# Kernel tuning notes

Measured on AMD Instinct MI355X. Metric: run time of the kernel, lower is better.

## Reference

```python
import jax, jax.numpy as jnp
import numpy as np

N = 4096      # number of nodes
C = 8         # channels (w1..w8 in source)
IN_DIM = 256  # input feature dim
D = 64        # per-channel dim (c_dim)
OUT = 128     # out_dim
ITERS = 4     # routing iterations
BETA = 1.0    # temperature
DENSITY = 0.01


def _l2norm(x):
    # tf.nn.l2_normalize along last axis with eps=1e-12
    return x * jax.lax.rsqrt(jnp.maximum(jnp.sum(x * x, axis=-1, keepdims=True), 1e-12))


def setup_inputs() -> dict:
    key = jax.random.key(0)
    k0, k1, k2, k3, k4, k5 = jax.random.split(key, 6)
    features = jax.random.normal(k0, (N, IN_DIM), dtype=jnp.float32)
    # sparse-ish 0/1 adjacency stored densely (as in the original model)
    adj = (jax.random.uniform(k1, (N, N)) < DENSITY).astype(jnp.float32)
    W = jax.random.normal(k2, (C, IN_DIM, D), dtype=jnp.float32)    # w1..w8 stacked
    b = jax.random.normal(k3, (C, 1, D), dtype=jnp.float32)         # b1..b8 stacked
    W_o = jax.random.normal(k4, (C * D, OUT), dtype=jnp.float32)
    bias = jax.random.normal(k5, (1, OUT), dtype=jnp.float32)
    return {"features": features, "adj": adj, "W": W, "b": b, "W_o": W_o, "bias": bias}


def reference(features, adj, W, b, W_o, bias):
    mask = adj > 0  # [N, N]
    # per-channel projection + l2 normalize: z[c] = l2norm(features @ w[c] + b[c])
    z = _l2norm(jnp.einsum('ni,cid->cnd', features, W) + b)  # [C, N, D]
    for _ in range(ITERS):
        # dense per-channel attention (XX^T), masked by adjacency
        A = jnp.einsum('cnd,cmd->cnm', z, z)                 # [C, N, N]
        A = jnp.where(mask[None], A, 0.0) / BETA
        # softmax across channels at each (i, j), then re-mask
        A = jax.nn.softmax(A, axis=0)
        A = jnp.where(mask[None], A, 0.0)
        # aggregate + residual + l2 normalize
        z = _l2norm(z + jnp.einsum('cnm,cmd->cnd', A, z))
    # concat channels along feature axis: [N, C*D]
    h = jnp.transpose(z, (1, 0, 2)).reshape(N, C * D)
    # (dropout skipped: stochastic op, identity in the deterministic reference)
    return h @ W_o + bias
```

## Files before the change

### kernel.cpp

```cpp
#include <hip/hip_runtime.h>
#include <hip/hip_bf16.h>

#define N_NODES 4096
#define C_CH    8
#define IN_DIM  256
#define D_DIM   64
#define CD      512
#define OUT_DIM 128
#define ITERS   4
#define STRIDE  128

typedef __hip_bfloat16 bf16;
typedef short short8 __attribute__((ext_vector_type(8)));
typedef float floatx4 __attribute__((ext_vector_type(4)));
typedef unsigned uintx4 __attribute__((ext_vector_type(4)));
typedef unsigned short ushortx4 __attribute__((ext_vector_type(4)));

__device__ __forceinline__ float bf2f(bf16 x) { return __bfloat162float(x); }

__device__ __forceinline__ unsigned f2b_rne(float x) {
    unsigned u = __float_as_uint(x);
    return (u + 0x7FFFu + ((u >> 16) & 1u)) >> 16;
}
__device__ __forceinline__ unsigned pack2bf(float a, float b) {
    return f2b_rne(a) | (f2b_rne(b) << 16);
}
__device__ __forceinline__ void unpack2(unsigned v, float& a, float& b) {
    a = __uint_as_float(v << 16);
    b = __uint_as_float(v & 0xFFFF0000u);
}
__device__ __forceinline__ short8 as_s8(uint4 u) {
    union { uint4 a; short8 b; } x; x.a = u; return x.b;
}

template<int CTRL>
__device__ __forceinline__ float dpp_add(float x) {
    int yi = __builtin_amdgcn_update_dpp(0, __float_as_int(x), CTRL, 0xF, 0xF, true);
    return x + __int_as_float(yi);
}

__device__ __forceinline__ bool wave_detect(const unsigned* __restrict__ feat_u) {
    int lane = threadIdx.x & 63;
    unsigned u = feat_u[lane];
    int e = (u >> 7) & 0xFF;
    int vote = (e >= 0x68 && e <= 0x86) ? 1 : 0;
    #pragma unroll
    for (int off = 32; off; off >>= 1) vote += __shfl_xor(vote, off);
    return vote >= 32;
}

__global__ __launch_bounds__(256) void stage_a(
        const void* __restrict__ feat, const void* __restrict__ W,
        const void* __restrict__ Wo,
        unsigned short* __restrict__ Wt, unsigned short* __restrict__ Wo_t) {
    bool isbf = wave_detect((const unsigned*)feat);
    int bx = blockIdx.x, t = threadIdx.x;
    if (bx < 8) {
        __shared__ __align__(16) unsigned short lt[IN_DIM * D_DIM];
        int c = bx;
        if (isbf) {
            const uint4* p = (const uint4*)((const unsigned short*)W + (size_t)c * IN_DIM * D_DIM);
            #pragma unroll
            for (int i = 0; i < 8; i++) {
                int idx = t + i * 256;
                *(uint4*)&lt[idx * 8] = p[idx];
            }
        } else {
            const float4* p = (const float4*)((const float*)W + (size_t)c * IN_DIM * D_DIM);
            #pragma unroll
            for (int i = 0; i < 16; i++) {
                int idx = t + i * 256;
                float4 f = p[idx];
                uint2 v = make_uint2(pack2bf(f.x, f.y), pack2bf(f.z, f.w));
                *(uint2*)&lt[idx * 4] = v;
            }
        }
        __syncthreads();
        uint4* wt4 = (uint4*)Wt;
        #pragma unroll
        for (int i = 0; i < 8; i++) {
            int j = t + i * 256;
            int d = j >> 5, seg = j & 31;
            int k0 = seg * 8;
            unsigned short v[8];
            #pragma unroll
            for (int k = 0; k < 8; k++) v[k] = lt[(k0 + k) * D_DIM + d];
            uint4 o;
            o.x = v[0] | ((unsigned)v[1] << 16);
            o.y = v[2] | ((unsigned)v[3] << 16);
            o.z = v[4] | ((unsigned)v[5] << 16);
            o.w = v[6] | ((unsigned)v[7] << 16);
            wt4[(c * 64 + d) * 32 + seg] = o;
        }
    } else {
        int base = (bx - 8) * 1024 + t * 4;
        #pragma unroll
        for (int q = 0; q < 4; q++) {
            int idx = base + q;
            int k = idx >> 7, n = idx & 127;
            unsigned short v;
            if (isbf) v = ((const unsigned short*)Wo)[idx];
            else      v = (unsigned short)f2b_rne(((const float*)Wo)[idx]);
            Wo_t[n * CD + k] = v;
        }
    }
}

__global__ __launch_bounds__(256) void stage_b(
        const void* __restrict__ feat, const void* __restrict__ adj,
        const void* __restrict__ b, const unsigned short* __restrict__ Wt,
        unsigned* __restrict__ zbf, int* __restrict__ deg,
        unsigned short* __restrict__ col_buf) {
    bool isbf = wave_detect((const unsigned*)feat);
    int bx = blockIdx.x, t = threadIdx.x;
    int w = t >> 6, lane = t & 63;
    __shared__ __align__(16) unsigned short zt[16 * CD];

    if (bx < 256) {
        int r0 = bx * 16;
        int n0 = w * 128;
        int m = lane & 15, quad = lane >> 4;
        int row = r0 + m;
        floatx4 acc[8];
        #pragma unroll
        for (int j = 0; j < 8; j++) acc[j] = (floatx4){0.f, 0.f, 0.f, 0.f};
        const uint4* wt4 = (const uint4*)Wt;

        if (isbf) {
            const uint4* a4 = (const uint4*)feat + (size_t)row * 32 + quad;
            #pragma unroll
            for (int k0 = 0; k0 < 8; k0++) {
                short8 a = as_s8(a4[k0 * 4]);
                #pragma unroll
                for (int j = 0; j < 8; j++) {
                    int col = n0 + j * 16 + m;
                    short8 bb = as_s8(wt4[col * 32 + k0 * 4 + quad]);
                    acc[j] = __builtin_amdgcn_mfma_f32_16x16x32_bf16(a, bb, acc[j], 0, 0, 0);
                }
            }
        } else {
            const float4* a4 = (const float4*)feat + (size_t)row * 64 + quad * 2;
            #pragma unroll
            for (int k0 = 0; k0 < 8; k0++) {
                float4 f0 = a4[k0 * 8], f1 = a4[k0 * 8 + 1];
                uint4 au;
                au.x = pack2bf(f0.x, f0.y); au.y = pack2bf(f0.z, f0.w);
                au.z = pack2bf(f1.x, f1.y); au.w = pack2bf(f1.z, f1.w);
                short8 a = as_s8(au);
                #pragma unroll
                for (int j = 0; j < 8; j++) {
                    int col = n0 + j * 16 + m;
                    short8 bb = as_s8(wt4[col * 32 + k0 * 4 + quad]);
                    acc[j] = __builtin_amdgcn_mfma_f32_16x16x32_bf16(a, bb, acc[j], 0, 0, 0);
                }
            }
        }

        float pre[8][4];
        #pragma unroll
        for (int j = 0; j < 8; j++) {
            int col = n0 + j * 16 + m;
            float bb = isbf ? bf2f(((const bf16*)b)[col]) : ((const float*)b)[col];
            #pragma unroll
            for (int r = 0; r < 4; r++) pre[j][r] = acc[j][r] + bb;
        }
        #pragma unroll
        for (int ch = 0; ch < 2; ch++) {
            float ss[4];
            #pragma unroll
            for (int r = 0; r < 4; r++) {
                float s = 0.f;
                #pragma unroll
                for (int jj = 0; jj < 4; jj++) {
                    float v = pre[ch * 4 + jj][r];
                    s = fmaf(v, v, s);
                }
                ss[r] = s;
            }
            #pragma unroll
            for (int off = 1; off < 16; off <<= 1) {
                #pragma unroll
                for (int r = 0; r < 4; r++) ss[r] += __shfl_xor(ss[r], off);
            }
            #pragma unroll
            for (int r = 0; r < 4; r++) {
                float sc = __builtin_amdgcn_rsqf(fmaxf(ss[r], 1e-12f));
                int lrow = quad * 4 + r;
                #pragma unroll
                for (int jj = 0; jj < 4; jj++) {
                    int j = ch * 4 + jj;
                    int col = n0 + j * 16 + m;
                    zt[lrow * CD + col] = (unsigned short)f2b_rne(pre[j][r] * sc);
                }
            }
        }
        __syncthreads();
        const uint4* zt4 = (const uint4*)zt;
        uint4* z4 = (uint4*)zbf;
        #pragma unroll
        for (int i = 0; i < 4; i++) {
            int j = t + i * 256;
            int lrow = j >> 6, seg = j & 63;
            z4[(size_t)(r0 + lrow) * 64 + seg] = zt4[j];
        }
    } else {
        int i = (bx - 256) * 4 + w;
        int base_out = i * STRIDE;
        int running = 0;
        int nch = isbf ? 8 : 16;
        for (int ch = 0; ch < nch; ch++) {
            unsigned bits = 0;
            int j0, nelem;
            if (isbf) {
                const uint4* p = (const uint4*)((const unsigned short*)adj + (size_t)i * N_NODES);
                uint4 u = p[ch * 64 + lane];
                j0 = (ch * 64 + lane) * 8; nelem = 8;
                unsigned short h[8] = {
                    (unsigned short)(u.x & 0xFFFF), (unsigned short)(u.x >> 16),
                    (unsigned short)(u.y & 0xFFFF), (unsigned short)(u.y >> 16),
                    (unsigned short)(u.z & 0xFFFF), (unsigned short)(u.z >> 16),
                    (unsigned short)(u.w & 0xFFFF), (unsigned short)(u.w >> 16)};
                #pragma unroll
                for (int k = 0; k < 8; k++)
                    if ((h[k] & 0x8000) == 0 && h[k] != 0) bits |= (1u << k);
            } else {
                const float4* p = (const float4*)((const float*)adj + (size_t)i * N_NODES);
                float4 f = p[ch * 64 + lane];
                j0 = (ch * 64 + lane) * 4; nelem = 4;
                if (f.x > 0.f) bits |= 1u;
                if (f.y > 0.f) bits |= 2u;
                if (f.z > 0.f) bits |= 4u;
                if (f.w > 0.f) bits |= 8u;
            }
            int cnt = __popc(bits);
            int sc = cnt;
            #pragma unroll
            for (int off = 1; off < 64; off <<= 1) {
                int v = __shfl_up(sc, off);
                if (lane >= off) sc += v;
            }
            int tot = __shfl(sc, 63);
            int pos = base_out + running + (sc - cnt);
            for (int k = 0; k < nelem; k++) {
                if ((bits >> k) & 1u) {
                    if (pos < base_out + STRIDE) col_buf[pos] = (unsigned short)(j0 + k);
                    pos++;
                }
            }
            running += tot;
        }
        if (lane == 0) deg[i] = (running < STRIDE) ? running : STRIDE;
    }
}

__device__ __forceinline__ void edge_step(const float zil2[8], float acc[8], uint4 u) {
    float vj[8];
    unpack2(u.x, vj[0], vj[1]);
    unpack2(u.y, vj[2], vj[3]);
    unpack2(u.z, vj[4], vj[5]);
    unpack2(u.w, vj[6], vj[7]);
    float p = 0.f;
    #pragma unroll
    for (int k = 0; k < 8; k++) p = fmaf(zil2[k], vj[k], p);
    p = dpp_add<0xB1>(p);
    p = dpp_add<0x4E>(p);
    p = dpp_add<0x141>(p);
    float ex = __builtin_amdgcn_exp2f(p);
    float s = dpp_add<0x128>(ex);
    s += __shfl_xor(s, 16);
    s += __shfl_xor(s, 32);
    float wgt = ex * __builtin_amdgcn_rcpf(s);
    #pragma unroll
    for (int k = 0; k < 8; k++) acc[k] = fmaf(wgt, vj[k], acc[k]);
}

__device__ __forceinline__ void finish_norm(float acc[8], float zi[8]) {
    float ss = 0.f;
    #pragma unroll
    for (int k = 0; k < 8; k++) ss = fmaf(acc[k], acc[k], ss);
    ss = dpp_add<0xB1>(ss);
    ss = dpp_add<0x4E>(ss);
    ss = dpp_add<0x141>(ss);
    float sc = __builtin_amdgcn_rsqf(fmaxf(ss, 1e-12f));
    #pragma unroll
    for (int k = 0; k < 8; k++) zi[k] = acc[k] * sc;
}

__global__ __launch_bounds__(256, 8) void route_iter(
        const unsigned* __restrict__ bin_u, unsigned* __restrict__ bot,
        const int* __restrict__ deg, const unsigned short* __restrict__ col_buf) {
    const float LOG2E = 1.4426950408889634f;
    int t = threadIdx.x;
    int w = t >> 6, lane = t & 63;
    int local = w >> 1;
    int half  = w & 1;
    int node = blockIdx.x * 2 + local;
    int g = lane >> 3, s = lane & 7;

    __shared__ __align__(16) unsigned short s_cols[2 * STRIDE];
    __shared__ __align__(16) float s_acc[2][CD];
    if (t < 128) {
        ((unsigned*)s_cols)[t] =
            ((const unsigned*)(col_buf + (size_t)blockIdx.x * (2 * STRIDE)))[t];
    }
    int dg = deg[node];
    __syncthreads();
    const unsigned short* mycols = s_cols + local * STRIDE;

    int frag = g * 32 + s * 4;
    unsigned fragb = (unsigned)frag << 2;

    uint4 uown = *(const uint4*)(bin_u + (size_t)node * 256 + frag);
    float zi[8], zil2[8], acc[8];
    unpack2(uown.x, zi[0], zi[1]); unpack2(uown.y, zi[2], zi[3]);
    unpack2(uown.z, zi[4], zi[5]); unpack2(uown.w, zi[6], zi[7]);
    #pragma unroll
    for (int k = 0; k < 8; k++) {
        zil2[k] = zi[k] * LOG2E;
        acc[k] = half ? 0.f : zi[k];
    }

    int h0 = ((dg >> 1) + 7) & ~7;
    if (h0 > dg) h0 = dg;
    int e   = half ? h0 : 0;
    int end = half ? dg : h0;

    const char* bin = (const char*)bin_u;
    for (; e + 3 < end; e += 4) {
        ushortx4 js = *(const ushortx4*)&mycols[e];
        uint4 u0 = *(const uint4*)(bin + (((unsigned)js.x << 10) + fragb));
        uint4 u1 = *(const uint4*)(bin + (((unsigned)js.y << 10) + fragb));
        uint4 u2 = *(const uint4*)(bin + (((unsigned)js.z << 10) + fragb));
        uint4 u3 = *(const uint4*)(bin + (((unsigned)js.w << 10) + fragb));
        edge_step(zil2, acc, u0);
        edge_step(zil2, acc, u1);
        edge_step(zil2, acc, u2);
        edge_step(zil2, acc, u3);
    }
    for (; e < end; e++) {
        unsigned j0 = mycols[e];
        uint4 u0 = *(const uint4*)(bin + ((j0 << 10) + fragb));
        edge_step(zil2, acc, u0);
    }

    int flat = g * D_DIM + s * 8;
    if (half) {
        *(float4*)&s_acc[local][flat]     = make_float4(acc[0], acc[1], acc[2], acc[3]);
        *(float4*)&s_acc[local][flat + 4] = make_float4(acc[4], acc[5], acc[6], acc[7]);
    }
    __syncthreads();
    if (!half) {
        float4 p0 = *(const float4*)&s_acc[local][flat];
        float4 p1 = *(const float4*)&s_acc[local][flat + 4];
        acc[0] += p0.x; acc[1] += p0.y; acc[2] += p0.z; acc[3] += p0.w;
        acc[4] += p1.x; acc[5] += p1.y; acc[6] += p1.z; acc[7] += p1.w;

        finish_norm(acc, zi);

        uintx4 ob;
        ob.x = pack2bf(zi[0], zi[1]); ob.y = pack2bf(zi[2], zi[3]);
        ob.z = pack2bf(zi[4], zi[5]); ob.w = pack2bf(zi[6], zi[7]);
        __builtin_nontemporal_store(
            ob, (uintx4*)(bot + (size_t)node * 256 + frag));
    }
}

__global__ __launch_bounds__(256) void out_gemm_mfma(
        const unsigned* __restrict__ zbf, const unsigned* __restrict__ wot_u,
        const void* __restrict__ bias, void* __restrict__ out,
        const void* __restrict__ feat) {
    bool isbf = wave_detect((const unsigned*)feat);
    int w = threadIdx.x >> 6, lane = threadIdx.x & 63;
    int r0 = blockIdx.x * 32 + (w & 1) * 16;
    int n0 = (w >> 1) * 64;
    int m = lane & 15, quad = lane >> 4;

    floatx4 acc0 = {0.f, 0.f, 0.f, 0.f}, acc1 = acc0, acc2 = acc0, acc3 = acc0;
    const unsigned* ap  = zbf   + (size_t)(r0 + m) * 256 + quad * 4;
    const unsigned* bp0 = wot_u + (size_t)(n0 + m) * 256 + quad * 4;
    const unsigned* bp1 = bp0 + 16 * 256;
    const unsigned* bp2 = bp0 + 32 * 256;
    const unsigned* bp3 = bp0 + 48 * 256;

    #pragma unroll
    for (int k0 = 0; k0 < 256; k0 += 16) {
        short8 a  = as_s8(*(const uint4*)(ap  + k0));
        short8 b0 = as_s8(*(const uint4*)(bp0 + k0));
        short8 b1 = as_s8(*(const uint4*)(bp1 + k0));
        short8 b2 = as_s8(*(const uint4*)(bp2 + k0));
        short8 b3 = as_s8(*(const uint4*)(bp3 + k0));
        acc0 = __builtin_amdgcn_mfma_f32_16x16x32_bf16(a, b0, acc0, 0, 0, 0);
        acc1 = __builtin_amdgcn_mfma_f32_16x16x32_bf16(a, b1, acc1, 0, 0, 0);
        acc2 = __builtin_amdgcn_mfma_f32_16x16x32_bf16(a, b2, acc2, 0, 0, 0);
        acc3 = __builtin_amdgcn_mfma_f32_16x16x32_bf16(a, b3, acc3, 0, 0, 0);
    }

    float accs[4][4] = {
        {acc0[0], acc0[1], acc0[2], acc0[3]},
        {acc1[0], acc1[1], acc1[2], acc1[3]},
        {acc2[0], acc2[1], acc2[2], acc2[3]},
        {acc3[0], acc3[1], acc3[2], acc3[3]}};
    #pragma unroll
    for (int c = 0; c < 4; c++) {
        int col = n0 + c * 16 + m;
        float bb = isbf ? bf2f(((const bf16*)bias)[col]) : ((const float*)bias)[col];
        #pragma unroll
        for (int r = 0; r < 4; r++) {
            int row = r0 + quad * 4 + r;
            float v = accs[c][r] + bb;
            size_t oi = (size_t)row * OUT_DIM + col;
            if (isbf) ((bf16*)out)[oi] = __float2bfloat16(v);
            else      ((float*)out)[oi] = v;
        }
    }
}

extern "C" void kernel_launch(void* const* d_in, const int* in_sizes, int n_in,
                              void* d_out, int out_size, void* d_ws, size_t ws_size,
                              hipStream_t stream) {
    const void* feat = d_in[0];
    const void* adj  = d_in[1];
    const void* W    = d_in[2];
    const void* b    = d_in[3];
    const void* Wo   = d_in[4];
    const void* bias = d_in[5];

    char* ws = (char*)d_ws;
    unsigned*       zbf_a   = (unsigned*)ws;
    unsigned*       zbf_b   = (unsigned*)(ws + (4u << 20));
    unsigned short* Wt      = (unsigned short*)(ws + (8u << 20));
    unsigned short* Wo_t    = (unsigned short*)(ws + (8u << 20) + (256u << 10));
    int*            deg     = (int*)(ws + (8u << 20) + (512u << 10));
    unsigned short* col_buf = (unsigned short*)(ws + (9u << 20));

    stage_a<<<72, 256, 0, stream>>>(feat, W, Wo, Wt, Wo_t);
    stage_b<<<1280, 256, 0, stream>>>(feat, adj, b, Wt, zbf_a, deg, col_buf);

    unsigned* bin = zbf_a;
    unsigned* bot = zbf_b;
    for (int it = 0; it < ITERS; it++) {
        route_iter<<<N_NODES / 2, 256, 0, stream>>>(bin, bot, deg, col_buf);
        unsigned* tb = bin; bin = bot; bot = tb;
    }

    out_gemm_mfma<<<N_NODES / 32, 256, 0, stream>>>(zbf_a, (const unsigned*)Wo_t,
                                                    bias, d_out, feat);
}
```

Measured before the change: 206.6 us.

## Fuse four routing iterations into one persistent kernel with a grid barrier

Replaces the four per-iteration route_iter launches with a single persistent kernel of 512 blocks. Each wave owns two nodes and runs all iterations, writing each iteration's output to its own buffer with write-through stores and meeting other blocks at a two-level atomic grid barrier. It drops the split of each node's edges across two waves and the shared-memory reduction between them, so each wave now walks a node's full edge list by itself. This removes launch gaps and the extra per-block reduction, but it relies on all blocks being co-resident, adds spin-wait cost at the barrier, and leaves less parallelism per node.

Result: slower. 222.1 us (+7.5%).

```diff
diff --git a/kernel.cpp b/kernel.cpp
--- a/kernel.cpp
+++ b/kernel.cpp
@@ -10,6 +10,16 @@
 #define ITERS   4
 #define STRIDE  128
 
+#define Z_STRIDE   (4u << 20)
+#define WT_OFF     (20u << 20)
+#define WOT_OFF    ((20u << 20) + (256u << 10))
+#define DEG_OFF    ((20u << 20) + (512u << 10))
+#define COL_OFF    (21u << 20)
+#define BAR_OFF    (22u << 20)
+
+#define RBLOCKS    512
+#define RGROUPS    32
+
 typedef __hip_bfloat16 bf16;
 typedef short short8 __attribute__((ext_vector_type(8)));
 typedef float floatx4 __attribute__((ext_vector_type(4)));
@@ -52,9 +62,15 @@
 __global__ __launch_bounds__(256) void stage_a(
         const void* __restrict__ feat, const void* __restrict__ W,
         const void* __restrict__ Wo,
-        unsigned short* __restrict__ Wt, unsigned short* __restrict__ Wo_t) {
+        unsigned short* __restrict__ Wt, unsigned short* __restrict__ Wo_t,
+        unsigned* __restrict__ bar) {
+    int bx = blockIdx.x, t = threadIdx.x;
+    if (bx == 72) {
+        #pragma unroll
+        for (int i = 0; i < 8; i++) bar[t + i * 256] = 0u;
+        return;
+    }
     bool isbf = wave_detect((const unsigned*)feat);
-    int bx = blockIdx.x, t = threadIdx.x;
     if (bx < 8) {
         __shared__ __align__(16) unsigned short lt[IN_DIM * D_DIM];
         int c = bx;
@@ -286,47 +302,16 @@
     for (int k = 0; k < 8; k++) zi[k] = acc[k] * sc;
 }
 
-__global__ __launch_bounds__(256, 8) void route_iter(
-        const unsigned* __restrict__ bin_u, unsigned* __restrict__ bot,
-        const int* __restrict__ deg, const unsigned short* __restrict__ col_buf) {
+__device__ __forceinline__ void route_node(
+        float zi[8], const unsigned short* mycols, int dg,
+        const char* bin, char* bout, int node, unsigned fragb, bool writethrough) {
     const float LOG2E = 1.4426950408889634f;
-    int t = threadIdx.x;
-    int w = t >> 6, lane = t & 63;
-    int local = w >> 1;
-    int half  = w & 1;
-    int node = blockIdx.x * 2 + local;
-    int g = lane >> 3, s = lane & 7;
-
-    __shared__ __align__(16) unsigned short s_cols[2 * STRIDE];
-    __shared__ __align__(16) float s_acc[2][CD];
-    if (t < 128) {
-        ((unsigned*)s_cols)[t] =
-            ((const unsigned*)(col_buf + (size_t)blockIdx.x * (2 * STRIDE)))[t];
-    }
-    int dg = deg[node];
-    __syncthreads();
-    const unsigned short* mycols = s_cols + local * STRIDE;
-
-    int frag = g * 32 + s * 4;
-    unsigned fragb = (unsigned)frag << 2;
-
-    uint4 uown = *(const uint4*)(bin_u + (size_t)node * 256 + frag);
-    float zi[8], zil2[8], acc[8];
-    unpack2(uown.x, zi[0], zi[1]); unpack2(uown.y, zi[2], zi[3]);
-    unpack2(uown.z, zi[4], zi[5]); unpack2(uown.w, zi[6], zi[7]);
-    #pragma unroll
-    for (int k = 0; k < 8; k++) {
-        zil2[k] = zi[k] * LOG2E;
-        acc[k] = half ? 0.f : zi[k];
-    }
-
-    int h0 = ((dg >> 1) + 7) & ~7;
-    if (h0 > dg) h0 = dg;
-    int e   = half ? h0 : 0;
-    int end = half ? dg : h0;
-
-    const char* bin = (const char*)bin_u;
-    for (; e + 3 < end; e += 4) {
+    float zil2[8], acc[8];
+    #pragma unroll
+    for (int k = 0; k < 8; k++) { zil2[k] = zi[k] * LOG2E; acc[k] = zi[k]; }
+
+    int e = 0;
+    for (; e + 3 < dg; e += 4) {
         ushortx4 js = *(const ushortx4*)&mycols[e];
         uint4 u0 = *(const uint4*)(bin + (((unsigned)js.x << 10) + fragb));
         uint4 u1 = *(const uint4*)(bin + (((unsigned)js.y << 10) + fragb));
@@ -337,31 +322,95 @@
         edge_step(zil2, acc, u2);
         edge_step(zil2, acc, u3);
     }
-    for (; e < end; e++) {
+    for (; e < dg; e++) {
         unsigned j0 = mycols[e];
         uint4 u0 = *(const uint4*)(bin + ((j0 << 10) + fragb));
         edge_step(zil2, acc, u0);
     }
 
-    int flat = g * D_DIM + s * 8;
-    if (half) {
-        *(float4*)&s_acc[local][flat]     = make_float4(acc[0], acc[1], acc[2], acc[3]);
-        *(float4*)&s_acc[local][flat + 4] = make_float4(acc[4], acc[5], acc[6], acc[7]);
-    }
+    finish_norm(acc, zi);
+
+    uintx4 ob;
+    ob.x = pack2bf(zi[0], zi[1]); ob.y = pack2bf(zi[2], zi[3]);
+    ob.z = pack2bf(zi[4], zi[5]); ob.w = pack2bf(zi[6], zi[7]);
+    char* p = bout + ((size_t)node << 10) + fragb;
+    if (writethrough) {
+        unsigned long long addr = (unsigned long long)(uintptr_t)p;
+        asm volatile("global_store_dwordx4 %0, %1, off sc0 sc1"
+                     :: "v"(addr), "v"(ob) : "memory");
+    } else {
+        *(uintx4*)p = ob;
+    }
+}
+
+__global__ __launch_bounds__(256, 2) void route_fused(
+        unsigned* __restrict__ zbase, const int* __restrict__ deg,
+        const unsigned short* __restrict__ col_buf, unsigned* __restrict__ bar) {
+    int t = threadIdx.x;
+    int w = t >> 6, lane = t & 63;
+    int b = blockIdx.x;
+    int g = lane >> 3, s = lane & 7;
+    int nA = b * 8 + w;
+    int nB = b * 8 + 4 + w;
+
+    __shared__ __align__(16) unsigned short s_cols[8 * STRIDE];
+    {
+        const unsigned* src = (const unsigned*)(col_buf + (size_t)b * 8 * STRIDE);
+        ((unsigned*)s_cols)[t]       = src[t];
+        ((unsigned*)s_cols)[t + 256] = src[t + 256];
+    }
+    int dgA = deg[nA], dgB = deg[nB];
     __syncthreads();
-    if (!half) {
-        float4 p0 = *(const float4*)&s_acc[local][flat];
-        float4 p1 = *(const float4*)&s_acc[local][flat + 4];
-        acc[0] += p0.x; acc[1] += p0.y; acc[2] += p0.z; acc[3] += p0.w;
-        acc[4] += p1.x; acc[5] += p1.y; acc[6] += p1.z; acc[7] += p1.w;
-
-        finish_norm(acc, zi);
-
-        uintx4 ob;
-        ob.x = pack2bf(zi[0], zi[1]); ob.y = pack2bf(zi[2], zi[3]);
-        ob.z = pack2bf(zi[4], zi[5]); ob.w = pack2bf(zi[6], zi[7]);
-        __builtin_nontemporal_store(
-            ob, (uintx4*)(bot + (size_t)node * 256 + frag));
+    const unsigned short* colsA = s_cols + w * STRIDE;
+    const unsigned short* colsB = s_cols + (4 + w) * STRIDE;
+
+    int frag = g * 32 + s * 4;
+    unsigned fragb = (unsigned)frag << 2;
+
+    uint4 ua = *(const uint4*)((const char*)zbase + ((size_t)nA << 10) + fragb);
+    uint4 ub = *(const uint4*)((const char*)zbase + ((size_t)nB << 10) + fragb);
+    float ziA[8], ziB[8];
+    unpack2(ua.x, ziA[0], ziA[1]); unpack2(ua.y, ziA[2], ziA[3]);
+    unpack2(ua.z, ziA[4], ziA[5]); unpack2(ua.w, ziA[6], ziA[7]);
+    unpack2(ub.x, ziB[0], ziB[1]); unpack2(ub.y, ziB[2], ziB[3]);
+    unpack2(ub.z, ziB[4], ziB[5]); unpack2(ub.w, ziB[6], ziB[7]);
+
+    for (int it = 0; it < ITERS; it++) {
+        const char* bin = (const char*)zbase + (size_t)it * Z_STRIDE;
+        char* bout = (char*)zbase + (size_t)(it + 1) * Z_STRIDE;
+        bool wt = (it != ITERS - 1);
+
+        route_node(ziA, colsA, dgA, bin, bout, nA, fragb, wt);
+        route_node(ziB, colsB, dgB, bin, bout, nB, fragb, wt);
+
+        if (it != ITERS - 1) {
+            __syncthreads();
+            if (t == 0) {
+                unsigned r1 = __hip_atomic_fetch_add(
+                        &bar[(b >> 4) * 32], 1u,
+                        __ATOMIC_RELAXED, __HIP_MEMORY_SCOPE_AGENT);
+                if ((r1 & 15u) == 15u) {
+                    unsigned r2 = __hip_atomic_fetch_add(
+                            &bar[RGROUPS * 32], 1u,
+                            __ATOMIC_RELAXED, __HIP_MEMORY_SCOPE_AGENT);
+                    if ((r2 & (RGROUPS - 1u)) == RGROUPS - 1u) {
+                        __hip_atomic_store(&bar[(RGROUPS + 1) * 32],
+                                           r2 / RGROUPS + 1u,
+                                           __ATOMIC_RELAXED,
+                                           __HIP_MEMORY_SCOPE_AGENT);
+                    }
+                }
+                unsigned target = (unsigned)(it + 1);
+                int tries = 0;
+                while (__hip_atomic_load(&bar[(RGROUPS + 1) * 32],
+                                         __ATOMIC_RELAXED,
+                                         __HIP_MEMORY_SCOPE_AGENT) < target) {
+                    __builtin_amdgcn_s_sleep(2);
+                    if (++tries > (1 << 18)) break;
+                }
+            }
+            __syncthreads();
+        }
     }
 }
 
@@ -426,23 +475,18 @@
     const void* bias = d_in[5];
 
     char* ws = (char*)d_ws;
-    unsigned*       zbf_a   = (unsigned*)ws;
-    unsigned*       zbf_b   = (unsigned*)(ws + (4u << 20));
-    unsigned short* Wt      = (unsigned short*)(ws + (8u << 20));
-    unsigned short* Wo_t    = (unsigned short*)(ws + (8u << 20) + (256u << 10));
-    int*            deg     = (int*)(ws + (8u << 20) + (512u << 10));
-    unsigned short* col_buf = (unsigned short*)(ws + (9u << 20));
-
-    stage_a<<<72, 256, 0, stream>>>(feat, W, Wo, Wt, Wo_t);
-    stage_b<<<1280, 256, 0, stream>>>(feat, adj, b, Wt, zbf_a, deg, col_buf);
-
-    unsigned* bin = zbf_a;
-    unsigned* bot = zbf_b;
-    for (int it = 0; it < ITERS; it++) {
-        route_iter<<<N_NODES / 2, 256, 0, stream>>>(bin, bot, deg, col_buf);
-        unsigned* tb = bin; bin = bot; bot = tb;
-    }
-
-    out_gemm_mfma<<<N_NODES / 32, 256, 0, stream>>>(zbf_a, (const unsigned*)Wo_t,
+    unsigned*       zbase   = (unsigned*)ws;
+    unsigned short* Wt      = (unsigned short*)(ws + WT_OFF);
+    unsigned short* Wo_t    = (unsigned short*)(ws + WOT_OFF);
+    int*            deg     = (int*)(ws + DEG_OFF);
+    unsigned short* col_buf = (unsigned short*)(ws + COL_OFF);
+    unsigned*       bar     = (unsigned*)(ws + BAR_OFF);
+
+    stage_a<<<73, 256, 0, stream>>>(feat, W, Wo, Wt, Wo_t, bar);
+    stage_b<<<1280, 256, 0, stream>>>(feat, adj, b, Wt, zbase, deg, col_buf);
+    route_fused<<<RBLOCKS, 256, 0, stream>>>(zbase, deg, col_buf, bar);
+
+    unsigned* z_final = (unsigned*)(ws + (size_t)ITERS * Z_STRIDE);
+    out_gemm_mfma<<<N_NODES / 32, 256, 0, stream>>>(z_final, (const unsigned*)Wo_t,
                                                     bias, d_out, feat);
 }
```
